# Kernel tuning notes

Hardware: AMD Instinct MI355X
Metric: run time of the kernel (lower is better)

The kernel has to match this reference:

```python
import jax, jax.numpy as jnp
import numpy as np

NUM_CLUSTERS = 16
CHANNELS = 256
UPDATE_RATE = 0.2
# channels % num_clusters == 0 -> all cluster capacities equal
_BASE = CHANNELS // NUM_CLUSTERS
_REM = CHANNELS % NUM_CLUSTERS
CLUSTER_SIZES = jnp.asarray([_BASE + 1] * _REM + [_BASE] * (NUM_CLUSTERS - _REM), dtype=jnp.int32)


def _cdist(a, b):
    # euclidean pairwise distance, batched over leading dims
    d2 = (jnp.sum(a * a, -1)[..., :, None]
          + jnp.sum(b * b, -1)[..., None, :]
          - 2.0 * (a @ jnp.swapaxes(b, -1, -2)))
    return jnp.sqrt(jnp.clip(d2, 0.0))


def _fps(D, k):
    # farthest point sampling given full [N,N] distance matrix
    start = jnp.argmax(D.sum(1))
    def step(min_d, _):
        far = jnp.argmax(min_d)
        return jnp.minimum(min_d, D[far]), far
    _, rest = jax.lax.scan(step, D[start], None, length=k - 1)
    return jnp.concatenate([start[None], rest])


def _capacity_assign(D, sizes):
    # greedy fixed-capacity assignment, sequential over channels
    order = jnp.argsort(D, axis=1)  # [C, K] cluster preference per channel
    def step(counts, row):
        avail = counts[row] < sizes[row]
        chosen = row[jnp.argmax(avail)]  # first available preference
        return counts.at[chosen].add(1), chosen
    _, assign = jax.lax.scan(step, jnp.zeros(sizes.shape[0], jnp.int32), order)
    return assign


def setup_inputs() -> dict:
    key = jax.random.key(0)
    k1, k2 = jax.random.split(key)
    features = jax.random.normal(k1, (8, CHANNELS, 64, 256), dtype=jnp.float32)
    pos_emb_batch = jax.random.normal(k2, (8, CHANNELS, 3), dtype=jnp.float32)
    return {"features": features, "pos_emb_batch": pos_emb_batch}


def reference(features, pos_emb_batch):
    b, c, nw, df = features.shape
    K = NUM_CLUSTERS
    pos = pos_emb_batch[0]                                   # [C, 3] (module's pos_emb buffer)
    # _initialize_centers: FPS over electrode positions
    centers = pos[_fps(_cdist(pos, pos), K)]                 # [K, 3]
    # _find_farthest_channels (euclidean): FPS over flattened features per batch
    ff = features.reshape(b, c, -1)
    Db = _cdist(ff, ff)                                      # [b, C, C]
    sel = jax.vmap(lambda D: _fps(D, K))(Db)                 # [b, K]
    # _cluster_euclidean_temp: nearest temp center per channel
    center_coords = pos_emb_batch[jnp.arange(b)[:, None], sel]      # [b, K, 3]
    temp_assign = jnp.argmin(_cdist(pos_emb_batch, center_coords), -1)  # [b, C]
    # per-cluster mean of positions over the whole batch
    flat_a = temp_assign.reshape(-1)
    flat_p = pos_emb_batch.reshape(-1, 3)
    sums = jax.ops.segment_sum(flat_p, flat_a, num_segments=K)
    cnts = jax.ops.segment_sum(jnp.ones(flat_a.shape, jnp.float32), flat_a, num_segments=K)
    avg = jnp.where(cnts[:, None] > 0, sums / jnp.maximum(cnts, 1.0)[:, None], 0.0)
    # match old centers to batch-average temp centers and EMA update
    matching = jnp.argmin(_cdist(centers, avg), axis=1)
    centers = (1.0 - UPDATE_RATE) * centers + UPDATE_RATE * avg[matching]
    # capacity-constrained final assignment
    return _capacity_assign(_cdist(pos, centers), CLUSTER_SIZES)
```

## Files before the change

kernel.cpp:

```cpp
#include <hip/hip_runtime.h>

#define NB 8
#define NC 256
#define DF 16384
#define KCL 16
#define SPLITS 16
#define KC (DF / SPLITS)
#define BK 32
#define ITERS (KC / BK)
#define NPAIR 3
#define GEMM_BLOCKS (NPAIR * 2 * NB * SPLITS)

typedef _Float16 half8 __attribute__((ext_vector_type(8)));
typedef _Float16 half4_t __attribute__((ext_vector_type(4)));
typedef float floatx4 __attribute__((ext_vector_type(4)));

__device__ const int TItab[NPAIR] = {0,0,1};
__device__ const int TJtab[NPAIR] = {0,1,1};

__device__ __forceinline__ int argmax256w(float v, float* sv, int* si) {
  int t = threadIdx.x;
  float bv = v; int bi = t;
  #pragma unroll
  for (int s = 32; s >= 1; s >>= 1) {
    float ov = __shfl_down(bv, s);
    int   oi = __shfl_down(bi, s);
    if (ov > bv || (ov == bv && oi < bi)) { bv = ov; bi = oi; }
  }
  int w = t >> 6;
  if ((t & 63) == 0) { sv[w] = bv; si[w] = bi; }
  __syncthreads();
  float rbv = sv[0]; int rbi = si[0];
  #pragma unroll
  for (int k = 1; k < 4; ++k) {
    float ov = sv[k]; int oi = si[k];
    if (ov > rbv || (ov == rbv && oi < rbi)) { rbv = ov; rbi = oi; }
  }
  __syncthreads();
  return rbi;
}

__global__ __launch_bounds__(256, 3) void k_gemm_pre(const float* __restrict__ ff,
                                                     const float* __restrict__ pe,
                                                     float* __restrict__ Pp,
                                                     float* __restrict__ centers0,
                                                     float* __restrict__ rs) {
  __shared__ _Float16 Ah[128][40];
  __shared__ _Float16 Al[128][40];
  __shared__ _Float16 Bh[64][40];
  __shared__ _Float16 Bl[64][40];

  const int bid = blockIdx.x;
  const int tid = threadIdx.x;

  if (bid == GEMM_BLOCKS) {
    float* sm = (float*)&Ah[0][0];
    float* px = sm;        float* py = sm + 256;
    float* pz = sm + 512;  float* pn = sm + 768;
    float* sv = sm + 1024; int*   si = (int*)(sm + 1280);
    int* fpsIdx = (int*)(sm + 1536);
    const int t = tid;
    for (int i = t; i < NB * NC; i += 256) rs[i] = 0.f;
    float x = pe[t * 3 + 0], y = pe[t * 3 + 1], z = pe[t * 3 + 2];
    float n = x * x + y * y + z * z;
    px[t] = x; py[t] = y; pz[t] = z; pn[t] = n;
    __syncthreads();
    float rsum = 0.f;
    for (int j = 0; j < NC; ++j) {
      float dot = x * px[j] + y * py[j] + z * pz[j];
      rsum += sqrtf(fmaxf(n + pn[j] - 2.f * dot, 0.f));
    }
    int start = argmax256w(rsum, sv, si);
    if (t == 0) fpsIdx[0] = start;
    float dot0 = x * px[start] + y * py[start] + z * pz[start];
    float mind = sqrtf(fmaxf(n + pn[start] - 2.f * dot0, 0.f));
    for (int it = 1; it < KCL; ++it) {
      int far = argmax256w(mind, sv, si);
      if (t == 0) fpsIdx[it] = far;
      float dot = x * px[far] + y * py[far] + z * pz[far];
      mind = fminf(mind, sqrtf(fmaxf(n + pn[far] - 2.f * dot, 0.f)));
    }
    __syncthreads();
    if (t < KCL) {
      int p = fpsIdx[t];
      centers0[t * 3 + 0] = px[p];
      centers0[t * 3 + 1] = py[p];
      centers0[t * 3 + 2] = pz[p];
    }
    return;
  }

  const int x    = bid & 7;
  const int slot = bid >> 3;
  const int tc   = slot % 6;
  const int u    = slot / 6;
  const int gi   = x * 16 + u;
  const int b    = gi & 7;
  const int sp   = gi >> 3;

  const int pair = tc >> 1, ch = tc & 1;
  const int ti = TItab[pair], tj = TJtab[pair];
  const bool diag = (ti == tj);

  const int wave = tid >> 6, lane = tid & 63;
  const int wr = wave >> 1, wc = wave & 1;
  const int lrow = lane & 15, q = lane >> 4;

  const int srA = tid >> 2, scA = (tid & 3) * 8;
  const int srB = tid >> 2, scB = (tid & 3) * 8;
  const float* gA0 = ff + ((size_t)(b * NC + ti * 128 + srA)) * DF + sp * KC + scA;
  const float* gA1 = gA0 + (size_t)64 * DF;
  const float* gB  = ff + ((size_t)(b * NC + tj * 128 + ch * 64 + srB)) * DF + sp * KC + scB;

  floatx4 a1[4][2], c23[4][2];
  #pragma unroll
  for (int i = 0; i < 4; ++i)
    #pragma unroll
    for (int j = 0; j < 2; ++j) { a1[i][j] = (floatx4)0.f; c23[i][j] = (floatx4)0.f; }

  float4 ra0 = *(const float4*)(gA0), ra1 = *(const float4*)(gA0 + 4);
  float4 ra2 = *(const float4*)(gA1), ra3 = *(const float4*)(gA1 + 4);
  float4 rb0 = make_float4(0.f, 0.f, 0.f, 0.f), rb1 = rb0;
  if (!diag) { rb0 = *(const float4*)(gB); rb1 = *(const float4*)(gB + 4); }
  gA0 += BK; gA1 += BK; gB += BK;

  for (int it = 0; it < ITERS; ++it) {
    half8 ah0, al0, ah1, al1;
    half8 bh8 = (half8)(_Float16)0.f, bl8 = (half8)(_Float16)0.f;
    {
      float f[8] = {ra0.x, ra0.y, ra0.z, ra0.w, ra1.x, ra1.y, ra1.z, ra1.w};
      #pragma unroll
      for (int e = 0; e < 8; ++e) {
        _Float16 h = (_Float16)f[e];
        ah0[e] = h; al0[e] = (_Float16)(f[e] - (float)h);
      }
    }
    {
      float f[8] = {ra2.x, ra2.y, ra2.z, ra2.w, ra3.x, ra3.y, ra3.z, ra3.w};
      #pragma unroll
      for (int e = 0; e < 8; ++e) {
        _Float16 h = (_Float16)f[e];
        ah1[e] = h; al1[e] = (_Float16)(f[e] - (float)h);
      }
    }
    if (!diag) {
      float f[8] = {rb0.x, rb0.y, rb0.z, rb0.w, rb1.x, rb1.y, rb1.z, rb1.w};
      #pragma unroll
      for (int e = 0; e < 8; ++e) {
        _Float16 h = (_Float16)f[e];
        bh8[e] = h; bl8[e] = (_Float16)(f[e] - (float)h);
      }
    }
    __syncthreads();
    *(half8*)&Ah[srA][scA] = ah0;
    *(half8*)&Al[srA][scA] = al0;
    *(half8*)&Ah[srA + 64][scA] = ah1;
    *(half8*)&Al[srA + 64][scA] = al1;
    if (!diag) {
      *(half8*)&Bh[srB][scB] = bh8;
      *(half8*)&Bl[srB][scB] = bl8;
    }
    __syncthreads();
    if (it + 1 < ITERS) {
      ra0 = *(const float4*)(gA0); ra1 = *(const float4*)(gA0 + 4);
      ra2 = *(const float4*)(gA1); ra3 = *(const float4*)(gA1 + 4);
      if (!diag) { rb0 = *(const float4*)(gB); rb1 = *(const float4*)(gB + 4); }
      gA0 += BK; gA1 += BK; gB += BK;
    }
    const _Float16* bhp = diag ? &Ah[ch * 64][0] : &Bh[0][0];
    const _Float16* blp = diag ? &Al[ch * 64][0] : &Bl[0][0];
    half8 bhf[2], blf[2];
    #pragma unroll
    for (int j = 0; j < 2; ++j) {
      bhf[j] = *(const half8*)(bhp + (wc * 32 + j * 16 + lrow) * 40 + q * 8);
      blf[j] = *(const half8*)(blp + (wc * 32 + j * 16 + lrow) * 40 + q * 8);
    }
    __builtin_amdgcn_s_setprio(1);
    #pragma unroll
    for (int i = 0; i < 4; ++i) {
      half8 a_h = *(const half8*)&Ah[wr * 64 + i * 16 + lrow][q * 8];
      half8 a_l = *(const half8*)&Al[wr * 64 + i * 16 + lrow][q * 8];
      #pragma unroll
      for (int j = 0; j < 2; ++j) {
        a1[i][j]  = __builtin_amdgcn_mfma_f32_16x16x32_f16(a_h, bhf[j], a1[i][j], 0, 0, 0);
        c23[i][j] = __builtin_amdgcn_mfma_f32_16x16x32_f16(a_h, blf[j], c23[i][j], 0, 0, 0);
        c23[i][j] = __builtin_amdgcn_mfma_f32_16x16x32_f16(a_l, bhf[j], c23[i][j], 0, 0, 0);
      }
    }
    __builtin_amdgcn_s_setprio(0);
  }

  float* Pb = Pp + (size_t)(sp * NB + b) * NC * NC;
  #pragma unroll
  for (int i = 0; i < 4; ++i) {
    int grow = ti * 128 + wr * 64 + i * 16 + q * 4;
    #pragma unroll
    for (int j = 0; j < 2; ++j) {
      int gcol = tj * 128 + ch * 64 + wc * 32 + j * 16 + lrow;
      float4 v;
      v.x = a1[i][j][0] + c23[i][j][0];
      v.y = a1[i][j][1] + c23[i][j][1];
      v.z = a1[i][j][2] + c23[i][j][2];
      v.w = a1[i][j][3] + c23[i][j][3];
      Pb[(size_t)(grow + 0) * NC + gcol] = v.x;
      Pb[(size_t)(grow + 1) * NC + gcol] = v.y;
      Pb[(size_t)(grow + 2) * NC + gcol] = v.z;
      Pb[(size_t)(grow + 3) * NC + gcol] = v.w;
      if (!diag) *(float4*)&Pb[(size_t)gcol * NC + grow] = v;
    }
  }
}

__global__ __launch_bounds__(256) void k_formD(const float* __restrict__ Pp,
                                               float* __restrict__ Db,
                                               float* __restrict__ rs) {
  __shared__ float dg_s[NC];
  const int t = threadIdx.x;
  const int b = blockIdx.x >> 5, i0 = (blockIdx.x & 31) * 8;
  float s = 0.f;
  #pragma unroll
  for (int sp = 0; sp < SPLITS; ++sp)
    s += Pp[((size_t)(sp * NB + b) * NC + t) * NC + t];
  dg_s[t] = s;
  __syncthreads();
  float colsum = 0.f;
  for (int ii = 0; ii < 8; ++ii) {
    int i = i0 + ii;
    float acc = 0.f;
    #pragma unroll
    for (int sp = 0; sp < SPLITS; ++sp)
      acc += Pp[((size_t)(sp * NB + b) * NC + i) * NC + t];
    float d2 = dg_s[i] + dg_s[t] - 2.f * acc;
    float d = sqrtf(fmaxf(d2, 0.f));
    Db[((size_t)b * NC + i) * NC + t] = d;
    colsum += d;
  }
  atomicAdd(&rs[b * NC + t], colsum);
}

__global__ __launch_bounds__(256) void k_fps_b(const float* __restrict__ Db,
                                               const float* __restrict__ rs,
                                               const float* __restrict__ pe,
                                               float* __restrict__ ccoord) {
  int b = blockIdx.x, t = threadIdx.x;
  const float* D = Db + (size_t)b * NC * NC;
  __shared__ float sv[4]; __shared__ int si[4];
  __shared__ int fpsIdx[KCL];
  int start = argmax256w(rs[b * NC + t], sv, si);
  if (t == 0) fpsIdx[0] = start;
  float mind = D[start * NC + t];
  for (int it = 1; it < KCL; ++it) {
    int far = argmax256w(mind, sv, si);
    if (t == 0) fpsIdx[it] = far;
    mind = fminf(mind, D[far * NC + t]);
  }
  __syncthreads();
  if (t < KCL) {
    int p = fpsIdx[t];
    ccoord[(b * KCL + t) * 3 + 0] = pe[(b * NC + p) * 3 + 0];
    ccoord[(b * KCL + t) * 3 + 1] = pe[(b * NC + p) * 3 + 1];
    ccoord[(b * KCL + t) * 3 + 2] = pe[(b * NC + p) * 3 + 2];
  }
}

__global__ __launch_bounds__(256) void k_final(const float* __restrict__ pe,
                                               const float* __restrict__ ccoord,
                                               const float* __restrict__ centers0,
                                               int* __restrict__ outp) {
  __shared__ float cc[NB * KCL * 3];
  __shared__ float cn[NB * KCL];
  __shared__ float sums[KCL][3];
  __shared__ int cnts[KCL];
  __shared__ float avg[KCL][3];
  __shared__ float an[KCL];
  __shared__ float c0[KCL * 3];
  __shared__ float c1x[KCL], c1y[KCL], c1z[KCL], c1n[KCL];
  __shared__ int order[NC][KCL];
  int t = threadIdx.x;
  for (int i = t; i < NB * KCL * 3; i += 256) cc[i] = ccoord[i];
  if (t < KCL * 3) c0[t] = centers0[t];
  if (t < KCL) { sums[t][0] = 0.f; sums[t][1] = 0.f; sums[t][2] = 0.f; cnts[t] = 0; }
  __syncthreads();
  if (t < NB * KCL) {
    float x = cc[t * 3], y = cc[t * 3 + 1], z = cc[t * 3 + 2];
    cn[t] = x * x + y * y + z * z;
  }
  __syncthreads();
  for (int b = 0; b < NB; ++b) {
    int p = b * NC + t;
    float x = pe[p * 3], y = pe[p * 3 + 1], z = pe[p * 3 + 2];
    float n = x * x + y * y + z * z;
    float best = 3.4e38f; int bi = 0;
    #pragma unroll
    for (int k = 0; k < KCL; ++k) {
      int c = b * KCL + k;
      float dot = x * cc[c * 3] + y * cc[c * 3 + 1] + z * cc[c * 3 + 2];
      float d2 = fmaxf(n + cn[c] - 2.f * dot, 0.f);
      if (d2 < best) { best = d2; bi = k; }
    }
    atomicAdd(&sums[bi][0], x);
    atomicAdd(&sums[bi][1], y);
    atomicAdd(&sums[bi][2], z);
    atomicAdd(&cnts[bi], 1);
  }
  __syncthreads();
  if (t < KCL) {
    float c = (float)cnts[t];
    float inv = 1.f / fmaxf(c, 1.f);
    float ax = (cnts[t] > 0) ? sums[t][0] * inv : 0.f;
    float ay = (cnts[t] > 0) ? sums[t][1] * inv : 0.f;
    float az = (cnts[t] > 0) ? sums[t][2] * inv : 0.f;
    avg[t][0] = ax; avg[t][1] = ay; avg[t][2] = az;
    an[t] = ax * ax + ay * ay + az * az;
  }
  __syncthreads();
  if (t < KCL) {
    float x = c0[t * 3], y = c0[t * 3 + 1], z = c0[t * 3 + 2];
    float n = x * x + y * y + z * z;
    float best = 3.4e38f; int bi = 0;
    #pragma unroll
    for (int j = 0; j < KCL; ++j) {
      float dot = x * avg[j][0] + y * avg[j][1] + z * avg[j][2];
      float d2 = fmaxf(n + an[j] - 2.f * dot, 0.f);
      if (d2 < best) { best = d2; bi = j; }
    }
    float nx = 0.8f * x + 0.2f * avg[bi][0];
    float ny = 0.8f * y + 0.2f * avg[bi][1];
    float nz = 0.8f * z + 0.2f * avg[bi][2];
    c1x[t] = nx; c1y[t] = ny; c1z[t] = nz;
    c1n[t] = nx * nx + ny * ny + nz * nz;
  }
  __syncthreads();
  {
    float x = pe[t * 3], y = pe[t * 3 + 1], z = pe[t * 3 + 2];
    float n = x * x + y * y + z * z;
    float v[KCL];
    #pragma unroll
    for (int k = 0; k < KCL; ++k) {
      float dot = x * c1x[k] + y * c1y[k] + z * c1z[k];
      v[k] = fmaxf(n + c1n[k] - 2.f * dot, 0.f);
    }
    bool used[KCL];
    #pragma unroll
    for (int k = 0; k < KCL; ++k) used[k] = false;
    for (int r = 0; r < KCL; ++r) {
      float best = 3.4e38f; int bi = 0;
      #pragma unroll
      for (int j = 0; j < KCL; ++j) {
        if (!used[j] && v[j] < best) { best = v[j]; bi = j; }
      }
      order[t][r] = bi;
      used[bi] = true;
    }
  }
  __syncthreads();
  if (t < 64) {
    int cnt = 0;
    int cur = (t < KCL) ? order[0][t] : 0;
    for (int i = 0; i < NC; ++i) {
      int nxt = (t < KCL && i + 1 < NC) ? order[i + 1][t] : 0;
      int ccur = __shfl(cnt, cur);
      bool avail = (t < KCL) && (ccur < 16);
      unsigned long long m = __ballot(avail);
      int chosen;
      if (m != 0ull) {
        int rank = __ffsll((unsigned long long)m) - 1;
        chosen = __shfl(cur, rank);
      } else {
        chosen = __shfl(cur, 0);
      }
      if (t == chosen) cnt++;
      if (t == 0) outp[i] = chosen;
      cur = nxt;
    }
  }
}

extern "C" void kernel_launch(void* const* d_in, const int* in_sizes, int n_in,
                              void* d_out, int out_size, void* d_ws, size_t ws_size,
                              hipStream_t stream) {
  (void)in_sizes; (void)n_in; (void)out_size; (void)ws_size;
  const float* features = (const float*)d_in[0];
  const float* pe = (const float*)d_in[1];
  char* ws = (char*)d_ws;
  float* Pp       = (float*)(ws);
  float* Db       = (float*)(ws + 33554432);
  float* rs       = (float*)(ws + 35651584);
  float* centers0 = (float*)(ws + 35659776);
  float* ccoord   = (float*)(ws + 35660288);
  int*   outp     = (int*)d_out;

  hipLaunchKernelGGL(k_gemm_pre, dim3(GEMM_BLOCKS + 1), dim3(256), 0, stream,
                     features, pe, Pp, centers0, rs);
  hipLaunchKernelGGL(k_formD, dim3(256), dim3(256), 0, stream, Pp, Db, rs);
  hipLaunchKernelGGL(k_fps_b, dim3(NB), dim3(256), 0, stream, Db, rs, pe, ccoord);
  hipLaunchKernelGGL(k_final, dim3(1), dim3(256), 0, stream, pe, ccoord, centers0, outp);
}
```

Before: 324.0 us.

## Load GEMM fragments straight from global into registers, dropping LDS staging

The split-fp16 GEMM loop no longer stages A and B tiles through shared memory. Each lane now loads its own MFMA fragment rows directly from global memory, converts them to hi/lo fp16 in registers, and prefetches the next K-slice. This removes both per-iteration __syncthreads and the LDS traffic. The cost is redundant global loads, since the same rows are fetched by several waves, plus higher register pressure, which is why launch bounds drop from 3 to 2 blocks per CU. The diagonal-tile reuse of A as B is also lost.

```diff
diff --git a/kernel.cpp b/kernel.cpp
--- a/kernel.cpp
+++ b/kernel.cpp
@@ -12,7 +12,6 @@
 #define GEMM_BLOCKS (NPAIR * 2 * NB * SPLITS)
 
 typedef _Float16 half8 __attribute__((ext_vector_type(8)));
-typedef _Float16 half4_t __attribute__((ext_vector_type(4)));
 typedef float floatx4 __attribute__((ext_vector_type(4)));
 
 __device__ const int TItab[NPAIR] = {0,0,1};
@@ -40,25 +39,31 @@
   return rbi;
 }
 
-__global__ __launch_bounds__(256, 3) void k_gemm_pre(const float* __restrict__ ff,
+__device__ __forceinline__ void cvt8(const float4& r0, const float4& r1,
+                                     half8& hh, half8& ll) {
+  float f[8] = {r0.x, r0.y, r0.z, r0.w, r1.x, r1.y, r1.z, r1.w};
+  #pragma unroll
+  for (int e = 0; e < 8; ++e) {
+    _Float16 h = (_Float16)f[e];
+    hh[e] = h; ll[e] = (_Float16)(f[e] - (float)h);
+  }
+}
+
+__global__ __launch_bounds__(256, 2) void k_gemm_pre(const float* __restrict__ ff,
                                                      const float* __restrict__ pe,
                                                      float* __restrict__ Pp,
                                                      float* __restrict__ centers0,
                                                      float* __restrict__ rs) {
-  __shared__ _Float16 Ah[128][40];
-  __shared__ _Float16 Al[128][40];
-  __shared__ _Float16 Bh[64][40];
-  __shared__ _Float16 Bl[64][40];
+  __shared__ float sm[1056];
 
   const int bid = blockIdx.x;
   const int tid = threadIdx.x;
 
   if (bid == GEMM_BLOCKS) {
-    float* sm = (float*)&Ah[0][0];
     float* px = sm;        float* py = sm + 256;
     float* pz = sm + 512;  float* pn = sm + 768;
-    float* sv = sm + 1024; int*   si = (int*)(sm + 1280);
-    int* fpsIdx = (int*)(sm + 1536);
+    float* sv = sm + 1024; int*   si = (int*)(sm + 1028);
+    int* fpsIdx = (int*)(sm + 1032);
     const int t = tid;
     for (int i = t; i < NB * NC; i += 256) rs[i] = 0.f;
     float x = pe[t * 3 + 0], y = pe[t * 3 + 1], z = pe[t * 3 + 2];
@@ -106,11 +111,16 @@
   const int wr = wave >> 1, wc = wave & 1;
   const int lrow = lane & 15, q = lane >> 4;
 
-  const int srA = tid >> 2, scA = (tid & 3) * 8;
-  const int srB = tid >> 2, scB = (tid & 3) * 8;
-  const float* gA0 = ff + ((size_t)(b * NC + ti * 128 + srA)) * DF + sp * KC + scA;
-  const float* gA1 = gA0 + (size_t)64 * DF;
-  const float* gB  = ff + ((size_t)(b * NC + tj * 128 + ch * 64 + srB)) * DF + sp * KC + scB;
+  const float* pA[4];
+  const float* pB[2];
+  #pragma unroll
+  for (int i = 0; i < 4; ++i)
+    pA[i] = ff + (size_t)(b * NC + ti * 128 + wr * 64 + i * 16 + lrow) * DF
+               + (size_t)sp * KC + q * 8;
+  #pragma unroll
+  for (int j = 0; j < 2; ++j)
+    pB[j] = ff + (size_t)(b * NC + tj * 128 + ch * 64 + wc * 32 + j * 16 + lrow) * DF
+               + (size_t)sp * KC + q * 8;
 
   floatx4 a1[4][2], c23[4][2];
   #pragma unroll
@@ -118,73 +128,50 @@
     #pragma unroll
     for (int j = 0; j < 2; ++j) { a1[i][j] = (floatx4)0.f; c23[i][j] = (floatx4)0.f; }
 
-  float4 ra0 = *(const float4*)(gA0), ra1 = *(const float4*)(gA0 + 4);
-  float4 ra2 = *(const float4*)(gA1), ra3 = *(const float4*)(gA1 + 4);
-  float4 rb0 = make_float4(0.f, 0.f, 0.f, 0.f), rb1 = rb0;
-  if (!diag) { rb0 = *(const float4*)(gB); rb1 = *(const float4*)(gB + 4); }
-  gA0 += BK; gA1 += BK; gB += BK;
+  float4 ra[4][2], rb[2][2];
+  #pragma unroll
+  for (int i = 0; i < 4; ++i) {
+    ra[i][0] = *(const float4*)(pA[i]);
+    ra[i][1] = *(const float4*)(pA[i] + 4);
+    pA[i] += BK;
+  }
+  #pragma unroll
+  for (int j = 0; j < 2; ++j) {
+    rb[j][0] = *(const float4*)(pB[j]);
+    rb[j][1] = *(const float4*)(pB[j] + 4);
+    pB[j] += BK;
+  }
 
   for (int it = 0; it < ITERS; ++it) {
-    half8 ah0, al0, ah1, al1;
-    half8 bh8 = (half8)(_Float16)0.f, bl8 = (half8)(_Float16)0.f;
-    {
-      float f[8] = {ra0.x, ra0.y, ra0.z, ra0.w, ra1.x, ra1.y, ra1.z, ra1.w};
+    half8 ah[4], al[4], bh[2], bl[2];
+    #pragma unroll
+    for (int i = 0; i < 4; ++i) cvt8(ra[i][0], ra[i][1], ah[i], al[i]);
+    #pragma unroll
+    for (int j = 0; j < 2; ++j) cvt8(rb[j][0], rb[j][1], bh[j], bl[j]);
+
+    if (it + 1 < ITERS) {
       #pragma unroll
-      for (int e = 0; e < 8; ++e) {
-        _Float16 h = (_Float16)f[e];
-        ah0[e] = h; al0[e] = (_Float16)(f[e] - (float)h);
-      }
-    }
-    {
-      float f[8] = {ra2.x, ra2.y, ra2.z, ra2.w, ra3.x, ra3.y, ra3.z, ra3.w};
-      #pragma unroll
-      for (int e = 0; e < 8; ++e) {
-        _Float16 h = (_Float16)f[e];
-        ah1[e] = h; al1[e] = (_Float16)(f[e] - (float)h);
-      }
-    }
-    if (!diag) {
-      float f[8] = {rb0.x, rb0.y, rb0.z, rb0.w, rb1.x, rb1.y, rb1.z, rb1.w};
-      #pragma unroll
-      for (int e = 0; e < 8; ++e) {
-        _Float16 h = (_Float16)f[e];
-        bh8[e] = h; bl8[e] = (_Float16)(f[e] - (float)h);
-      }
-    }
-    __syncthreads();
-    *(half8*)&Ah[srA][scA] = ah0;
-    *(half8*)&Al[srA][scA] = al0;
-    *(half8*)&Ah[srA + 64][scA] = ah1;
-    *(half8*)&Al[srA + 64][scA] = al1;
-    if (!diag) {
-      *(half8*)&Bh[srB][scB] = bh8;
-      *(half8*)&Bl[srB][scB] = bl8;
-    }
-    __syncthreads();
-    if (it + 1 < ITERS) {
-      ra0 = *(const float4*)(gA0); ra1 = *(const float4*)(gA0 + 4);
-      ra2 = *(const float4*)(gA1); ra3 = *(const float4*)(gA1 + 4);
-      if (!diag) { rb0 = *(const float4*)(gB); rb1 = *(const float4*)(gB + 4); }
-      gA0 += BK; gA1 += BK; gB += BK;
-    }
-    const _Float16* bhp = diag ? &Ah[ch * 64][0] : &Bh[0][0];
-    const _Float16* blp = diag ? &Al[ch * 64][0] : &Bl[0][0];
-    half8 bhf[2], blf[2];
-    #pragma unroll
-    for (int j = 0; j < 2; ++j) {
-      bhf[j] = *(const half8*)(bhp + (wc * 32 + j * 16 + lrow) * 40 + q * 8);
-      blf[j] = *(const half8*)(blp + (wc * 32 + j * 16 + lrow) * 40 + q * 8);
-    }
-    __builtin_amdgcn_s_setprio(1);
-    #pragma unroll
-    for (int i = 0; i < 4; ++i) {
-      half8 a_h = *(const half8*)&Ah[wr * 64 + i * 16 + lrow][q * 8];
-      half8 a_l = *(const half8*)&Al[wr * 64 + i * 16 + lrow][q * 8];
+      for (int i = 0; i < 4; ++i) {
+        ra[i][0] = *(const float4*)(pA[i]);
+        ra[i][1] = *(const float4*)(pA[i] + 4);
+        pA[i] += BK;
+      }
       #pragma unroll
       for (int j = 0; j < 2; ++j) {
-        a1[i][j]  = __builtin_amdgcn_mfma_f32_16x16x32_f16(a_h, bhf[j], a1[i][j], 0, 0, 0);
-        c23[i][j] = __builtin_amdgcn_mfma_f32_16x16x32_f16(a_h, blf[j], c23[i][j], 0, 0, 0);
-        c23[i][j] = __builtin_amdgcn_mfma_f32_16x16x32_f16(a_l, bhf[j], c23[i][j], 0, 0, 0);
+        rb[j][0] = *(const float4*)(pB[j]);
+        rb[j][1] = *(const float4*)(pB[j] + 4);
+        pB[j] += BK;
+      }
+    }
+
+    __builtin_amdgcn_s_setprio(1);
+    #pragma unroll
+    for (int i = 0; i < 4; ++i) {
+      #pragma unroll
+      for (int j = 0; j < 2; ++j) {
+        a1[i][j]  = __builtin_amdgcn_mfma_f32_16x16x32_f16(ah[i], bh[j], a1[i][j], 0, 0, 0);
+        c23[i][j] = __builtin_amdgcn_mfma_f32_16x16x32_f16(ah[i], bl[j], c23[i][j], 0, 0, 0);
+        c23[i][j] = __builtin_amdgcn_mfma_f32_16x16x32_f16(al[i], bh[j], c23[i][j], 0, 0, 0);
       }
     }
     __builtin_amdgcn_s_setprio(0);
```

After: 374.0 us. 1.15x slower.
